# Kernel tuning notes

Measured on AMD Instinct MI355X. Metric: run time of the kernel, lower is better.

Reference implementation:

```python
import jax, jax.numpy as jnp
import numpy as np

NUM_EMBEDDINGS = 1024
EMBEDDING_DIM = 64
BETA = 0.25
N_TOKENS = 131072


def setup_inputs() -> dict:
    key = jax.random.key(0)
    k_z, k_cb = jax.random.split(key)
    z = jax.random.normal(k_z, (N_TOKENS, EMBEDDING_DIM), dtype=jnp.float32)
    # nn.Embedding weight initialized uniform(-1/K, 1/K)
    codebook = jax.random.uniform(
        k_cb, (NUM_EMBEDDINGS, EMBEDDING_DIM), dtype=jnp.float32,
        minval=-1.0 / NUM_EMBEDDINGS, maxval=1.0 / NUM_EMBEDDINGS)
    return {"z": z, "codebook": codebook}


def reference(z, codebook):
    # z: [N, D], codebook: [K, D]
    z_flat = z.reshape(-1, z.shape[-1])
    # squared euclidean distances: ||z||^2 - 2 z.E^T + ||E||^2 -> [N, K]
    distances = (jnp.sum(z_flat * z_flat, axis=1, keepdims=True)
                 - 2.0 * jnp.einsum('nd,kd->nk', z_flat, codebook)
                 + jnp.sum(codebook * codebook, axis=1))
    indices = jnp.argmin(distances, axis=1)          # [N]
    z_q = codebook[indices].reshape(z.shape)          # [N, D]
    # commitment + codebook losses
    loss = (BETA * jnp.mean((jax.lax.stop_gradient(z_q) - z) ** 2)
            + jnp.mean((z_q - jax.lax.stop_gradient(z)) ** 2))
    # straight-through estimator
    z_q_st = z + jax.lax.stop_gradient(z_q - z)
    return z_q_st, loss
```

## Files before the change

### kernel.cpp

```cpp
#include <hip/hip_runtime.h>


typedef __attribute__((ext_vector_type(8))) short bf16x8;
typedef __attribute__((ext_vector_type(4))) float f32x4;

#define N_TOKENS 131072
#define DIM 64
#define DYN_LDS 135168

__device__ __forceinline__ short f32_bf16(float f) {
  unsigned u = __builtin_bit_cast(unsigned, f);
  unsigned r = u + 0x7FFFu + ((u >> 16) & 1u);
  return (short)(r >> 16);
}

__global__ __launch_bounds__(256) void vq_prep(
    const float* __restrict__ cb, unsigned short* __restrict__ ch,
    float* __restrict__ ca2) {
  const int lane = threadIdx.x & 63;
  const int wv = threadIdx.x >> 6;
  const int code = blockIdx.x * 4 + wv;
  const float e = cb[code * DIM + lane] * 1024.0f;
  ch[code * DIM + lane] = (unsigned short)f32_bf16(e);
  float sq = e * e;
  #pragma unroll
  for (int w = 32; w >= 1; w >>= 1) sq += __shfl_xor(sq, w, 64);
  if (lane == 0) ca2[code] = 128.0f - sq * (1.0f / 2048.0f);
}

__global__ __launch_bounds__(512, 2) void vq_argmin(
    const float* __restrict__ z, const unsigned short* __restrict__ ch,
    const float* __restrict__ ca2, const float* __restrict__ cb,
    float* __restrict__ out, double* __restrict__ part) {
  extern __shared__ char lds[];
  unsigned short* Bs = (unsigned short*)lds;
  float* ca_s = (float*)(lds + 131072);
  __shared__ double sml[8];

  const int tid = threadIdx.x, lane = tid & 63, wv = tid >> 6;
  const int g = lane >> 4, c15 = lane & 15, sw = c15 & 7;
  const size_t wrow = (size_t)blockIdx.x * 512 + (size_t)wv * 64;
  const unsigned kmask = 0xFFFFFC00u;

  #pragma unroll
  for (int q = 0; q < 16; ++q) {
    const int chunk = q * 512 + tid;
    const int code = chunk >> 3, c = chunk & 7;
    __builtin_amdgcn_global_load_lds(
        (const __attribute__((address_space(1))) unsigned int*)
            (ch + code * DIM + ((c ^ (code & 7)) << 3)),
        (__attribute__((address_space(3))) unsigned int*)(Bs + chunk * 8),
        16, 0, 0);
  }
  if (tid < 256)
    __builtin_amdgcn_global_load_lds(
        (const __attribute__((address_space(1))) unsigned int*)(ca2 + tid * 4),
        (__attribute__((address_space(3))) unsigned int*)(ca_s + tid * 4),
        16, 0, 0);

  f32x4 a0[2][2][2];
  const float* zb = z + wrow * DIM;
  #pragma unroll
  for (int m = 0; m < 2; ++m)
    #pragma unroll
    for (int kk = 0; kk < 2; ++kk) {
      const float* p = zb + (m * 16 + c15) * DIM + kk * 32 + g * 8;
      a0[m][kk][0] = *(const f32x4*)p;
      a0[m][kk][1] = *(const f32x4*)(p + 4);
    }

  __syncthreads();

  float zsq = 0.0f;
  auto convA = [&](f32x4 (&ar)[2][2][2], bf16x8 (&ah)[2][2]) {
    #pragma unroll
    for (int m = 0; m < 2; ++m)
      #pragma unroll
      for (int kk = 0; kk < 2; ++kk)
        #pragma unroll
        for (int j = 0; j < 4; ++j) {
          const float v0 = ar[m][kk][0][j], v1 = ar[m][kk][1][j];
          ah[m][kk][j]     = f32_bf16(v0);
          ah[m][kk][j + 4] = f32_bf16(v1);
          zsq += v0 * v0 + v1 * v1;
        }
  };

  auto sweep_epi = [&](bf16x8 (&ah)[2][2], int p) -> float {
    unsigned best[2][4];
    #pragma unroll
    for (int m = 0; m < 2; ++m)
      #pragma unroll
      for (int r = 0; r < 4; ++r) best[m][r] = 0u;
    const char* bsp = (const char*)Bs;
    const int bx0 = ((0 * 4 + g) ^ sw) << 4;
    const int bx1 = ((1 * 4 + g) ^ sw) << 4;
    #pragma unroll 2
    for (int t = 0; t < 32; ++t) {
      bf16x8 bf[2][2];
      #pragma unroll
      for (int n = 0; n < 2; ++n) {
        const int rowb = (t * 32 + n * 16 + c15) * 128;
        bf[n][0] = *(const bf16x8*)(bsp + rowb + bx0);
        bf[n][1] = *(const bf16x8*)(bsp + rowb + bx1);
      }
      #pragma unroll
      for (int n = 0; n < 2; ++n) {
        const float can = ca_s[t * 32 + n * 16 + c15];
        const f32x4 cv = {can, can, can, can};
        const unsigned cc = 1023u - (unsigned)(t * 32 + n * 16 + c15);
        #pragma unroll
        for (int m = 0; m < 2; ++m) {
          f32x4 acc = __builtin_amdgcn_mfma_f32_16x16x32_bf16(
              ah[m][0], bf[n][0], cv, 0, 0, 0);
          acc = __builtin_amdgcn_mfma_f32_16x16x32_bf16(
              ah[m][1], bf[n][1], acc, 0, 0, 0);
          #pragma unroll
          for (int r = 0; r < 4; ++r) {
            const unsigned key =
                (__builtin_bit_cast(unsigned, acc[r]) & kmask) | cc;
            best[m][r] = key > best[m][r] ? key : best[m][r];
          }
        }
      }
    }
    float lossx = 0.0f;
    const f32x4* cb4 = (const f32x4*)cb;
    f32x4* out4 = (f32x4*)out;
    #pragma unroll
    for (int m = 0; m < 2; ++m)
      #pragma unroll
      for (int r = 0; r < 4; ++r) {
        unsigned bk = best[m][r];
        #pragma unroll
        for (int w = 1; w < 16; w <<= 1) {
          const unsigned ob = (unsigned)__shfl_xor((int)bk, w, 64);
          bk = ob > bk ? ob : bk;
        }
        const int row = p * 32 + m * 16 + g * 4 + r;
        const int bi = 1023 - (int)(bk & 1023u);
        out4[(wrow + row) * 16 + c15] = cb4[bi * 16 + c15];
        if (c15 == 0) lossx += 128.0f - __builtin_bit_cast(float, bk & kmask);
      }
    return lossx;
  };

  bf16x8 ah[2][2];
  convA(a0, ah);
  f32x4 a1[2][2][2];
  #pragma unroll
  for (int m = 0; m < 2; ++m)
    #pragma unroll
    for (int kk = 0; kk < 2; ++kk) {
      const float* p = zb + (32 + m * 16 + c15) * DIM + kk * 32 + g * 8;
      a1[m][kk][0] = *(const f32x4*)p;
      a1[m][kk][1] = *(const f32x4*)(p + 4);
    }
  float lossx = sweep_epi(ah, 0);

  convA(a1, ah);
  lossx += sweep_epi(ah, 1);

  float psum = zsq + lossx * (1.0f / 512.0f);
  #pragma unroll
  for (int w = 32; w >= 1; w >>= 1) psum += __shfl_xor(psum, w, 64);
  if (lane == 0) sml[wv] = (double)psum;
  __syncthreads();
  if (tid == 0) {
    double t = 0.0;
    #pragma unroll
    for (int i = 0; i < 8; ++i) t += sml[i];
    part[blockIdx.x] = t;
  }
}

__global__ __launch_bounds__(256) void vq_finalize(
    const double* __restrict__ part, float* __restrict__ out_loss) {
  __shared__ double s[4];
  const int tid = threadIdx.x, lane = tid & 63, wv = tid >> 6;
  double v = part[tid];
  #pragma unroll
  for (int w = 32; w >= 1; w >>= 1) v += __shfl_xor(v, w, 64);
  if (lane == 0) s[wv] = v;
  __syncthreads();
  if (tid == 0)
    out_loss[0] = (float)(1.25 * (s[0] + s[1] + s[2] + s[3]) /
                          ((double)N_TOKENS * (double)DIM));
}

extern "C" void kernel_launch(void* const* d_in, const int* in_sizes, int n_in,
                              void* d_out, int out_size, void* d_ws, size_t ws_size,
                              hipStream_t stream) {
  const float* z = (const float*)d_in[0];
  const float* cb = (const float*)d_in[1];
  float* out = (float*)d_out;
  char* ws = (char*)d_ws;

  unsigned short* ch = (unsigned short*)(ws);
  float* ca2 = (float*)(ws + 131072);
  double* part = (double*)(ws + 135168);

  (void)hipFuncSetAttribute((const void*)vq_argmin,
                            hipFuncAttributeMaxDynamicSharedMemorySize, DYN_LDS);

  vq_prep<<<256, 256, 0, stream>>>(cb, ch, ca2);
  vq_argmin<<<256, 512, DYN_LDS, stream>>>(z, ch, ca2, cb, out, part);
  vq_finalize<<<1, 256, 0, stream>>>(part, out + (size_t)N_TOKENS * DIM);
}
```

Before: 35.54 us.

## Fuse codebook prep and loss finalize into single argmin kernel

Removes the separate codebook-prep and finalize kernels: each block now converts the fp32 codebook to swizzled bf16 in LDS itself and computes code norms, and the last block (detected via an atomic counter) reduces the partial losses. The per-wave token tile is processed in one pass of 64 rows (4 m-tiles) instead of two 32-row sweeps, halving LDS B-fragment reads per token. It adds a memset launch and redundant per-block codebook conversion, plus higher register pressure from 16 best keys and 4x2 A fragments.

```diff
diff --git a/kernel.cpp b/kernel.cpp
--- a/kernel.cpp
+++ b/kernel.cpp
@@ -14,178 +14,163 @@
   return (short)(r >> 16);
 }
 
-__global__ __launch_bounds__(256) void vq_prep(
-    const float* __restrict__ cb, unsigned short* __restrict__ ch,
-    float* __restrict__ ca2) {
-  const int lane = threadIdx.x & 63;
-  const int wv = threadIdx.x >> 6;
-  const int code = blockIdx.x * 4 + wv;
-  const float e = cb[code * DIM + lane] * 1024.0f;
-  ch[code * DIM + lane] = (unsigned short)f32_bf16(e);
-  float sq = e * e;
-  #pragma unroll
-  for (int w = 32; w >= 1; w >>= 1) sq += __shfl_xor(sq, w, 64);
-  if (lane == 0) ca2[code] = 128.0f - sq * (1.0f / 2048.0f);
-}
-
-__global__ __launch_bounds__(512, 2) void vq_argmin(
-    const float* __restrict__ z, const unsigned short* __restrict__ ch,
-    const float* __restrict__ ca2, const float* __restrict__ cb,
-    float* __restrict__ out, double* __restrict__ part) {
+__global__ __launch_bounds__(512, 2) void vq_fused(
+    const float* __restrict__ z, const float* __restrict__ cb,
+    float* __restrict__ out, double* __restrict__ part,
+    unsigned* __restrict__ cnt) {
   extern __shared__ char lds[];
   unsigned short* Bs = (unsigned short*)lds;
   float* ca_s = (float*)(lds + 131072);
-  __shared__ double sml[8];
+  __shared__ float sml[8];
+  __shared__ int lastflag;
+  __shared__ double swav[8];
 
   const int tid = threadIdx.x, lane = tid & 63, wv = tid >> 6;
   const int g = lane >> 4, c15 = lane & 15, sw = c15 & 7;
   const size_t wrow = (size_t)blockIdx.x * 512 + (size_t)wv * 64;
   const unsigned kmask = 0xFFFFFC00u;
 
-  #pragma unroll
-  for (int q = 0; q < 16; ++q) {
-    const int chunk = q * 512 + tid;
-    const int code = chunk >> 3, c = chunk & 7;
-    __builtin_amdgcn_global_load_lds(
-        (const __attribute__((address_space(1))) unsigned int*)
-            (ch + code * DIM + ((c ^ (code & 7)) << 3)),
-        (__attribute__((address_space(3))) unsigned int*)(Bs + chunk * 8),
-        16, 0, 0);
-  }
-  if (tid < 256)
-    __builtin_amdgcn_global_load_lds(
-        (const __attribute__((address_space(1))) unsigned int*)(ca2 + tid * 4),
-        (__attribute__((address_space(3))) unsigned int*)(ca_s + tid * 4),
-        16, 0, 0);
-
-  f32x4 a0[2][2][2];
+  f32x4 a[4][2][2];
   const float* zb = z + wrow * DIM;
   #pragma unroll
-  for (int m = 0; m < 2; ++m)
+  for (int m = 0; m < 4; ++m)
     #pragma unroll
     for (int kk = 0; kk < 2; ++kk) {
       const float* p = zb + (m * 16 + c15) * DIM + kk * 32 + g * 8;
-      a0[m][kk][0] = *(const f32x4*)p;
-      a0[m][kk][1] = *(const f32x4*)(p + 4);
+      a[m][kk][0] = *(const f32x4*)p;
+      a[m][kk][1] = *(const f32x4*)(p + 4);
     }
 
+  #pragma unroll
+  for (int cc = 0; cc < 2; ++cc) {
+    const int code = tid + cc * 512;
+    const f32x4* src = (const f32x4*)(cb + code * DIM);
+    float sq = 0.0f;
+    #pragma unroll
+    for (int c = 0; c < 8; ++c) {
+      const f32x4 u = src[c * 2], v = src[c * 2 + 1];
+      bf16x8 w;
+      #pragma unroll
+      for (int j = 0; j < 4; ++j) {
+        const float e0 = u[j] * 1024.0f;
+        const float e1 = v[j] * 1024.0f;
+        w[j]     = f32_bf16(e0);
+        w[j + 4] = f32_bf16(e1);
+        sq += e0 * e0 + e1 * e1;
+      }
+      *(bf16x8*)((char*)Bs + code * 128 + ((c ^ (code & 7)) << 4)) = w;
+    }
+    ca_s[code] = 128.0f - sq * (1.0f / 2048.0f);
+  }
   __syncthreads();
 
+  bf16x8 ah[4][2];
   float zsq = 0.0f;
-  auto convA = [&](f32x4 (&ar)[2][2][2], bf16x8 (&ah)[2][2]) {
+  #pragma unroll
+  for (int m = 0; m < 4; ++m)
     #pragma unroll
-    for (int m = 0; m < 2; ++m)
+    for (int kk = 0; kk < 2; ++kk)
       #pragma unroll
-      for (int kk = 0; kk < 2; ++kk)
+      for (int j = 0; j < 4; ++j) {
+        const float v0 = a[m][kk][0][j], v1 = a[m][kk][1][j];
+        ah[m][kk][j]     = f32_bf16(v0);
+        ah[m][kk][j + 4] = f32_bf16(v1);
+        zsq += v0 * v0 + v1 * v1;
+      }
+
+  unsigned best[4][4];
+  #pragma unroll
+  for (int m = 0; m < 4; ++m)
+    #pragma unroll
+    for (int r = 0; r < 4; ++r) best[m][r] = 0u;
+
+  const char* bsp = (const char*)Bs;
+  const int bx0 = (g ^ sw) << 4;
+  const int bx1 = ((4 + g) ^ sw) << 4;
+
+  #pragma unroll 2
+  for (int t = 0; t < 32; ++t) {
+    bf16x8 bf[2][2];
+    #pragma unroll
+    for (int n = 0; n < 2; ++n) {
+      const int rowb = (t * 32 + n * 16 + c15) * 128;
+      bf[n][0] = *(const bf16x8*)(bsp + rowb + bx0);
+      bf[n][1] = *(const bf16x8*)(bsp + rowb + bx1);
+    }
+    #pragma unroll
+    for (int n = 0; n < 2; ++n) {
+      const float can = ca_s[t * 32 + n * 16 + c15];
+      const f32x4 cv = {can, can, can, can};
+      const unsigned cc = 1023u - (unsigned)(t * 32 + n * 16 + c15);
+      #pragma unroll
+      for (int m = 0; m < 4; ++m) {
+        f32x4 acc = __builtin_amdgcn_mfma_f32_16x16x32_bf16(
+            ah[m][0], bf[n][0], cv, 0, 0, 0);
+        acc = __builtin_amdgcn_mfma_f32_16x16x32_bf16(
+            ah[m][1], bf[n][1], acc, 0, 0, 0);
         #pragma unroll
-        for (int j = 0; j < 4; ++j) {
-          const float v0 = ar[m][kk][0][j], v1 = ar[m][kk][1][j];
-          ah[m][kk][j]     = f32_bf16(v0);
-          ah[m][kk][j + 4] = f32_bf16(v1);
-          zsq += v0 * v0 + v1 * v1;
-        }
-  };
-
-  auto sweep_epi = [&](bf16x8 (&ah)[2][2], int p) -> float {
-    unsigned best[2][4];
-    #pragma unroll
-    for (int m = 0; m < 2; ++m)
-      #pragma unroll
-      for (int r = 0; r < 4; ++r) best[m][r] = 0u;
-    const char* bsp = (const char*)Bs;
-    const int bx0 = ((0 * 4 + g) ^ sw) << 4;
-    const int bx1 = ((1 * 4 + g) ^ sw) << 4;
-    #pragma unroll 2
-    for (int t = 0; t < 32; ++t) {
-      bf16x8 bf[2][2];
-      #pragma unroll
-      for (int n = 0; n < 2; ++n) {
-        const int rowb = (t * 32 + n * 16 + c15) * 128;
-        bf[n][0] = *(const bf16x8*)(bsp + rowb + bx0);
-        bf[n][1] = *(const bf16x8*)(bsp + rowb + bx1);
-      }
-      #pragma unroll
-      for (int n = 0; n < 2; ++n) {
-        const float can = ca_s[t * 32 + n * 16 + c15];
-        const f32x4 cv = {can, can, can, can};
-        const unsigned cc = 1023u - (unsigned)(t * 32 + n * 16 + c15);
-        #pragma unroll
-        for (int m = 0; m < 2; ++m) {
-          f32x4 acc = __builtin_amdgcn_mfma_f32_16x16x32_bf16(
-              ah[m][0], bf[n][0], cv, 0, 0, 0);
-          acc = __builtin_amdgcn_mfma_f32_16x16x32_bf16(
-              ah[m][1], bf[n][1], acc, 0, 0, 0);
-          #pragma unroll
-          for (int r = 0; r < 4; ++r) {
-            const unsigned key =
-                (__builtin_bit_cast(unsigned, acc[r]) & kmask) | cc;
-            best[m][r] = key > best[m][r] ? key : best[m][r];
-          }
+        for (int r = 0; r < 4; ++r) {
+          const unsigned key =
+              (__builtin_bit_cast(unsigned, acc[r]) & kmask) | cc;
+          best[m][r] = key > best[m][r] ? key : best[m][r];
         }
       }
     }
-    float lossx = 0.0f;
-    const f32x4* cb4 = (const f32x4*)cb;
-    f32x4* out4 = (f32x4*)out;
+  }
+
+  float lossx = 0.0f;
+  const f32x4* cb4 = (const f32x4*)cb;
+  f32x4* out4 = (f32x4*)out;
+  #pragma unroll
+  for (int m = 0; m < 4; ++m)
     #pragma unroll
-    for (int m = 0; m < 2; ++m)
+    for (int r = 0; r < 4; ++r) {
+      unsigned bk = best[m][r];
       #pragma unroll
-      for (int r = 0; r < 4; ++r) {
-        unsigned bk = best[m][r];
-        #pragma unroll
-        for (int w = 1; w < 16; w <<= 1) {
-          const unsigned ob = (unsigned)__shfl_xor((int)bk, w, 64);
-          bk = ob > bk ? ob : bk;
-        }
-        const int row = p * 32 + m * 16 + g * 4 + r;
-        const int bi = 1023 - (int)(bk & 1023u);
-        out4[(wrow + row) * 16 + c15] = cb4[bi * 16 + c15];
-        if (c15 == 0) lossx += 128.0f - __builtin_bit_cast(float, bk & kmask);
+      for (int w = 1; w < 16; w <<= 1) {
+        const unsigned ob = (unsigned)__shfl_xor((int)bk, w, 64);
+        bk = ob > bk ? ob : bk;
       }
-    return lossx;
-  };
-
-  bf16x8 ah[2][2];
-  convA(a0, ah);
-  f32x4 a1[2][2][2];
-  #pragma unroll
-  for (int m = 0; m < 2; ++m)
-    #pragma unroll
-    for (int kk = 0; kk < 2; ++kk) {
-      const float* p = zb + (32 + m * 16 + c15) * DIM + kk * 32 + g * 8;
-      a1[m][kk][0] = *(const f32x4*)p;
-      a1[m][kk][1] = *(const f32x4*)(p + 4);
+      const int row = m * 16 + g * 4 + r;
+      const int bi = 1023 - (int)(bk & 1023u);
+      out4[(wrow + row) * 16 + c15] = cb4[bi * 16 + c15];
+      if (c15 == 0) lossx += 128.0f - __builtin_bit_cast(float, bk & kmask);
     }
-  float lossx = sweep_epi(ah, 0);
-
-  convA(a1, ah);
-  lossx += sweep_epi(ah, 1);
 
   float psum = zsq + lossx * (1.0f / 512.0f);
   #pragma unroll
   for (int w = 32; w >= 1; w >>= 1) psum += __shfl_xor(psum, w, 64);
-  if (lane == 0) sml[wv] = (double)psum;
+  if (lane == 0) sml[wv] = psum;
   __syncthreads();
   if (tid == 0) {
     double t = 0.0;
     #pragma unroll
-    for (int i = 0; i < 8; ++i) t += sml[i];
-    part[blockIdx.x] = t;
+    for (int i = 0; i < 8; ++i) t += (double)sml[i];
+    __hip_atomic_store(&part[blockIdx.x], t, __ATOMIC_RELEASE,
+                       __HIP_MEMORY_SCOPE_AGENT);
+    const unsigned old = __hip_atomic_fetch_add(cnt, 1u, __ATOMIC_ACQ_REL,
+                                                __HIP_MEMORY_SCOPE_AGENT);
+    lastflag = (old == 255u);
   }
-}
+  __syncthreads();
 
-__global__ __launch_bounds__(256) void vq_finalize(
-    const double* __restrict__ part, float* __restrict__ out_loss) {
-  __shared__ double s[4];
-  const int tid = threadIdx.x, lane = tid & 63, wv = tid >> 6;
-  double v = part[tid];
-  #pragma unroll
-  for (int w = 32; w >= 1; w >>= 1) v += __shfl_xor(v, w, 64);
-  if (lane == 0) s[wv] = v;
-  __syncthreads();
-  if (tid == 0)
-    out_loss[0] = (float)(1.25 * (s[0] + s[1] + s[2] + s[3]) /
-                          ((double)N_TOKENS * (double)DIM));
+  if (lastflag) {
+    double v = 0.0;
+    if (tid < 256)
+      v = __hip_atomic_load(&part[tid], __ATOMIC_ACQUIRE,
+                            __HIP_MEMORY_SCOPE_AGENT);
+    #pragma unroll
+    for (int w = 32; w >= 1; w >>= 1) v += __shfl_xor(v, w, 64);
+    if (lane == 0) swav[wv] = v;
+    __syncthreads();
+    if (tid == 0) {
+      double s = 0.0;
+      #pragma unroll
+      for (int i = 0; i < 8; ++i) s += swav[i];
+      out[(size_t)N_TOKENS * DIM] =
+          (float)(1.25 * s / ((double)N_TOKENS * (double)DIM));
+    }
+  }
 }
 
 extern "C" void kernel_launch(void* const* d_in, const int* in_sizes, int n_in,
@@ -196,14 +181,12 @@
   float* out = (float*)d_out;
   char* ws = (char*)d_ws;
 
-  unsigned short* ch = (unsigned short*)(ws);
-  float* ca2 = (float*)(ws + 131072);
-  double* part = (double*)(ws + 135168);
+  unsigned* cnt = (unsigned*)(ws);
+  double* part = (double*)(ws + 8);
 
-  (void)hipFuncSetAttribute((const void*)vq_argmin,
+  (void)hipFuncSetAttribute((const void*)vq_fused,
                             hipFuncAttributeMaxDynamicSharedMemorySize, DYN_LDS);
 
-  vq_prep<<<256, 256, 0, stream>>>(cb, ch, ca2);
-  vq_argmin<<<256, 512, DYN_LDS, stream>>>(z, ch, ca2, cb, out, part);
-  vq_finalize<<<1, 256, 0, stream>>>(part, out + (size_t)N_TOKENS * DIM);
+  hipMemsetAsync(cnt, 0, sizeof(unsigned), stream);
+  vq_fused<<<256, 512, DYN_LDS, stream>>>(z, cb, out, part, cnt);
 }
```

New measurement: 72.57 us. 104% more time.

## Sweep codebook once for all 64 rows with software-pipelined LDS loads

Applied to the files above, without the earlier changes.

Instead of two separate codebook sweeps over 32-row halves, each wave converts all 64 token rows to bf16 up front and sweeps the LDS codebook once. Every B fragment loaded from LDS is reused across four M tiles, halving LDS read traffic. B fragments are double-buffered so the next tile's loads overlap the current MFMAs. This raises register pressure (more A fragments and best keys live at once), which could hurt occupancy under the 512x2 launch bounds.

```diff
diff --git a/kernel.cpp b/kernel.cpp
--- a/kernel.cpp
+++ b/kernel.cpp
@@ -35,7 +35,7 @@
   extern __shared__ char lds[];
   unsigned short* Bs = (unsigned short*)lds;
   float* ca_s = (float*)(lds + 131072);
-  __shared__ double sml[8];
+  __shared__ float sml[8];
 
   const int tid = threadIdx.x, lane = tid & 63, wv = tid >> 6;
   const int g = lane >> 4, c15 = lane & 15, sw = c15 & 7;
@@ -71,105 +71,120 @@
 
   __syncthreads();
 
-  float zsq = 0.0f;
-  auto convA = [&](f32x4 (&ar)[2][2][2], bf16x8 (&ah)[2][2]) {
-    #pragma unroll
-    for (int m = 0; m < 2; ++m)
-      #pragma unroll
-      for (int kk = 0; kk < 2; ++kk)
-        #pragma unroll
-        for (int j = 0; j < 4; ++j) {
-          const float v0 = ar[m][kk][0][j], v1 = ar[m][kk][1][j];
-          ah[m][kk][j]     = f32_bf16(v0);
-          ah[m][kk][j + 4] = f32_bf16(v1);
-          zsq += v0 * v0 + v1 * v1;
-        }
-  };
-
-  auto sweep_epi = [&](bf16x8 (&ah)[2][2], int p) -> float {
-    unsigned best[2][4];
-    #pragma unroll
-    for (int m = 0; m < 2; ++m)
-      #pragma unroll
-      for (int r = 0; r < 4; ++r) best[m][r] = 0u;
-    const char* bsp = (const char*)Bs;
-    const int bx0 = ((0 * 4 + g) ^ sw) << 4;
-    const int bx1 = ((1 * 4 + g) ^ sw) << 4;
-    #pragma unroll 2
-    for (int t = 0; t < 32; ++t) {
-      bf16x8 bf[2][2];
-      #pragma unroll
-      for (int n = 0; n < 2; ++n) {
-        const int rowb = (t * 32 + n * 16 + c15) * 128;
-        bf[n][0] = *(const bf16x8*)(bsp + rowb + bx0);
-        bf[n][1] = *(const bf16x8*)(bsp + rowb + bx1);
-      }
-      #pragma unroll
-      for (int n = 0; n < 2; ++n) {
-        const float can = ca_s[t * 32 + n * 16 + c15];
-        const f32x4 cv = {can, can, can, can};
-        const unsigned cc = 1023u - (unsigned)(t * 32 + n * 16 + c15);
-        #pragma unroll
-        for (int m = 0; m < 2; ++m) {
-          f32x4 acc = __builtin_amdgcn_mfma_f32_16x16x32_bf16(
-              ah[m][0], bf[n][0], cv, 0, 0, 0);
-          acc = __builtin_amdgcn_mfma_f32_16x16x32_bf16(
-              ah[m][1], bf[n][1], acc, 0, 0, 0);
-          #pragma unroll
-          for (int r = 0; r < 4; ++r) {
-            const unsigned key =
-                (__builtin_bit_cast(unsigned, acc[r]) & kmask) | cc;
-            best[m][r] = key > best[m][r] ? key : best[m][r];
-          }
-        }
-      }
-    }
-    float lossx = 0.0f;
-    const f32x4* cb4 = (const f32x4*)cb;
-    f32x4* out4 = (f32x4*)out;
-    #pragma unroll
-    for (int m = 0; m < 2; ++m)
-      #pragma unroll
-      for (int r = 0; r < 4; ++r) {
-        unsigned bk = best[m][r];
-        #pragma unroll
-        for (int w = 1; w < 16; w <<= 1) {
-          const unsigned ob = (unsigned)__shfl_xor((int)bk, w, 64);
-          bk = ob > bk ? ob : bk;
-        }
-        const int row = p * 32 + m * 16 + g * 4 + r;
-        const int bi = 1023 - (int)(bk & 1023u);
-        out4[(wrow + row) * 16 + c15] = cb4[bi * 16 + c15];
-        if (c15 == 0) lossx += 128.0f - __builtin_bit_cast(float, bk & kmask);
-      }
-    return lossx;
-  };
-
-  bf16x8 ah[2][2];
-  convA(a0, ah);
   f32x4 a1[2][2][2];
   #pragma unroll
   for (int m = 0; m < 2; ++m)
     #pragma unroll
     for (int kk = 0; kk < 2; ++kk) {
-      const float* p = zb + (32 + m * 16 + c15) * DIM + kk * 32 + g * 8;
+      const float* p = zb + ((m + 2) * 16 + c15) * DIM + kk * 32 + g * 8;
       a1[m][kk][0] = *(const f32x4*)p;
       a1[m][kk][1] = *(const f32x4*)(p + 4);
     }
-  float lossx = sweep_epi(ah, 0);
-
-  convA(a1, ah);
-  lossx += sweep_epi(ah, 1);
+
+  bf16x8 ah[4][2];
+  float zsq = 0.0f;
+  #pragma unroll
+  for (int m = 0; m < 2; ++m)
+    #pragma unroll
+    for (int kk = 0; kk < 2; ++kk)
+      #pragma unroll
+      for (int j = 0; j < 4; ++j) {
+        const float v0 = a0[m][kk][0][j], v1 = a0[m][kk][1][j];
+        ah[m][kk][j]     = f32_bf16(v0);
+        ah[m][kk][j + 4] = f32_bf16(v1);
+        zsq += v0 * v0 + v1 * v1;
+      }
+  #pragma unroll
+  for (int m = 0; m < 2; ++m)
+    #pragma unroll
+    for (int kk = 0; kk < 2; ++kk)
+      #pragma unroll
+      for (int j = 0; j < 4; ++j) {
+        const float v0 = a1[m][kk][0][j], v1 = a1[m][kk][1][j];
+        ah[m + 2][kk][j]     = f32_bf16(v0);
+        ah[m + 2][kk][j + 4] = f32_bf16(v1);
+        zsq += v0 * v0 + v1 * v1;
+      }
+
+  unsigned best[4][4];
+  #pragma unroll
+  for (int m = 0; m < 4; ++m)
+    #pragma unroll
+    for (int r = 0; r < 4; ++r) best[m][r] = 0u;
+
+  const char* bsp = (const char*)Bs;
+  const int bx0 = (g ^ sw) << 4;
+  const int bx1 = ((4 + g) ^ sw) << 4;
+
+  auto LDB = [&](int t, bf16x8& b00, bf16x8& b01, bf16x8& b10, bf16x8& b11) {
+    const int r0 = (t * 32 + c15) * 128;
+    b00 = *(const bf16x8*)(bsp + r0 + bx0);
+    b01 = *(const bf16x8*)(bsp + r0 + bx1);
+    b10 = *(const bf16x8*)(bsp + r0 + 2048 + bx0);
+    b11 = *(const bf16x8*)(bsp + r0 + 2048 + bx1);
+  };
+  auto MM = [&](int t, bf16x8 b00, bf16x8 b01, bf16x8 b10, bf16x8 b11) {
+    #pragma unroll
+    for (int n = 0; n < 2; ++n) {
+      const bf16x8 f0 = n ? b10 : b00;
+      const bf16x8 f1 = n ? b11 : b01;
+      const float can = ca_s[t * 32 + n * 16 + c15];
+      const f32x4 cv = {can, can, can, can};
+      const unsigned cc = 1023u - (unsigned)(t * 32 + n * 16 + c15);
+      #pragma unroll
+      for (int m = 0; m < 4; ++m) {
+        f32x4 acc = __builtin_amdgcn_mfma_f32_16x16x32_bf16(
+            ah[m][0], f0, cv, 0, 0, 0);
+        acc = __builtin_amdgcn_mfma_f32_16x16x32_bf16(
+            ah[m][1], f1, acc, 0, 0, 0);
+        #pragma unroll
+        for (int r = 0; r < 4; ++r) {
+          const unsigned key =
+              (__builtin_bit_cast(unsigned, acc[r]) & kmask) | cc;
+          best[m][r] = key > best[m][r] ? key : best[m][r];
+        }
+      }
+    }
+  };
+
+  bf16x8 x00, x01, x10, x11, y00, y01, y10, y11;
+  LDB(0, x00, x01, x10, x11);
+  #pragma unroll 1
+  for (int t2 = 0; t2 < 16; ++t2) {
+    LDB(t2 * 2 + 1, y00, y01, y10, y11);
+    MM(t2 * 2, x00, x01, x10, x11);
+    LDB((t2 * 2 + 2) & 31, x00, x01, x10, x11);
+    MM(t2 * 2 + 1, y00, y01, y10, y11);
+  }
+
+  float lossx = 0.0f;
+  const f32x4* cb4 = (const f32x4*)cb;
+  f32x4* out4 = (f32x4*)out;
+  #pragma unroll
+  for (int m = 0; m < 4; ++m)
+    #pragma unroll
+    for (int r = 0; r < 4; ++r) {
+      unsigned bk = best[m][r];
+      #pragma unroll
+      for (int w = 1; w < 16; w <<= 1) {
+        const unsigned ob = (unsigned)__shfl_xor((int)bk, w, 64);
+        bk = ob > bk ? ob : bk;
+      }
+      const int row = m * 16 + g * 4 + r;
+      const int bi = 1023 - (int)(bk & 1023u);
+      out4[(wrow + row) * 16 + c15] = cb4[bi * 16 + c15];
+      if (c15 == 0) lossx += 128.0f - __builtin_bit_cast(float, bk & kmask);
+    }
 
   float psum = zsq + lossx * (1.0f / 512.0f);
   #pragma unroll
   for (int w = 32; w >= 1; w >>= 1) psum += __shfl_xor(psum, w, 64);
-  if (lane == 0) sml[wv] = (double)psum;
+  if (lane == 0) sml[wv] = psum;
   __syncthreads();
   if (tid == 0) {
     double t = 0.0;
     #pragma unroll
-    for (int i = 0; i < 8; ++i) t += sml[i];
+    for (int i = 0; i < 8; ++i) t += (double)sml[i];
     part[blockIdx.x] = t;
   }
 }
```

Result: no change. 34.96 us (-1.6%).
